# Kernel tuning notes

Hardware: AMD Instinct MI355X
Metric: run time of the kernel (lower is better)

## Reference

```python
import jax, jax.numpy as jnp
import numpy as np

DIM = 1024
NUM_HEADS = 16
HEAD_DIM = DIM // NUM_HEADS


def setup_inputs() -> dict:
    key = jax.random.key(0)
    k_x, k_q, k_k, k_v, k_o = jax.random.split(key, 5)
    B, L = 2, 2048
    scale = 1.0 / np.sqrt(DIM)
    x_bld = jax.random.normal(k_x, (B, L, DIM), dtype=jnp.float32)
    # LinearGeneral kernels: (in_features, num_heads, head_dim) for q/k/v,
    # (num_heads, head_dim, out_features) for out. Init ~ lecun_normal-ish scale.
    Wq = jax.random.normal(k_q, (DIM, NUM_HEADS, HEAD_DIM), dtype=jnp.float32) * scale
    Wk = jax.random.normal(k_k, (DIM, NUM_HEADS, HEAD_DIM), dtype=jnp.float32) * scale
    Wv = jax.random.normal(k_v, (DIM, NUM_HEADS, HEAD_DIM), dtype=jnp.float32) * scale
    Wo = jax.random.normal(k_o, (NUM_HEADS, HEAD_DIM, DIM), dtype=jnp.float32) * scale
    return {"x_bld": x_bld, "Wq": Wq, "Wk": Wk, "Wv": Wv, "Wo": Wo}


def reference(x_bld, Wq, Wk, Wv, Wo) -> jnp.ndarray:
    # Projections: [B,L,D] x [D,H,hd] -> [B,L,H,hd]
    q_blhd = jnp.einsum('bld,dhk->blhk', x_bld, Wq)
    k_blhd = jnp.einsum('bld,dhk->blhk', x_bld, Wk)
    v_blhd = jnp.einsum('bld,dhk->blhk', x_bld, Wv)
    # Scores: [B,H,L,L]
    attn_bhll = jnp.einsum('bqhd,bkhd->bhqk', q_blhd, k_blhd)
    attn_bhll = attn_bhll / jnp.sqrt(jnp.asarray(HEAD_DIM, dtype=attn_bhll.dtype))
    L = x_bld.shape[1]
    qi = jnp.arange(L)[:, None]
    ki = jnp.arange(L)[None, :]
    mask_ll = ki <= qi  # causal, no window
    neg_inf = jnp.finfo(attn_bhll.dtype).min
    attn_bhll = jnp.where(mask_ll[None, None, :, :], attn_bhll, neg_inf)
    attn_bhll = jax.nn.softmax(attn_bhll, axis=-1)
    y_blhd = jnp.einsum('bhqk,bkhd->bqhd', attn_bhll, v_blhd)
    # Output projection: contract (H, hd) -> D
    return jnp.einsum('blhk,hkd->bld', y_blhd, Wo)
```

## Files before the change

### kernel.cpp

```cpp
#include <hip/hip_runtime.h>
#include <hip/hip_bf16.h>

typedef __hip_bfloat16 bf16;
typedef __attribute__((ext_vector_type(8))) short short8;
typedef __attribute__((ext_vector_type(4))) float f32x4;

__device__ __forceinline__ float bfbits2f(unsigned short u) {
    return __uint_as_float(((unsigned int)u) << 16);
}
__device__ __forceinline__ unsigned short f2bfbits(float f) {
    union { float f; unsigned int u; } x;
    x.f = f;
    unsigned int r = x.u + 0x7FFFu + ((x.u >> 16) & 1u);
    return (unsigned short)(r >> 16);
}
__device__ __forceinline__ void async_copy16(const void* g, void* l) {
    __builtin_amdgcn_global_load_lds(
        (const __attribute__((address_space(1))) void*)g,
        (__attribute__((address_space(3))) void*)l, 16, 0, 0);
}

__global__ __launch_bounds__(256) void detect_dtype(
    const unsigned int* __restrict__ p0, const unsigned int* __restrict__ p1,
    const unsigned int* __restrict__ p2, const unsigned int* __restrict__ p3,
    const unsigned int* __restrict__ p4, int* __restrict__ flags) {
    const unsigned int* ps[5] = {p0, p1, p2, p3, p4};
    const unsigned int* p = ps[blockIdx.x];
    const int tid = threadIdx.x;
    int cnt = 0;
    for (int i = tid; i < 4096; i += 256) {
        unsigned int e = (p[i] >> 7) & 0xFFu;
        cnt += (e >= 90u && e <= 150u) ? 1 : 0;
    }
    __shared__ int r[256];
    r[tid] = cnt;
    __syncthreads();
    for (int off = 128; off; off >>= 1) {
        if (tid < off) r[tid] += r[tid + off];
        __syncthreads();
    }
    if (tid == 0) flags[blockIdx.x] = (r[0] > 2048) ? 1 : 0;
}

__global__ __launch_bounds__(256) void conv_x(const void* __restrict__ X,
                                              short* __restrict__ xb,
                                              const int* __restrict__ flags) {
    const bool isBf = flags[0] != 0;
    const int i = (blockIdx.x * 256 + threadIdx.x) * 8;
    if (isBf) {
        *(short8*)&xb[i] = *(const short8*)((const short*)X + i);
    } else {
        const float* xf = (const float*)X + i;
        float4 a = *(const float4*)xf;
        float4 b = *(const float4*)(xf + 4);
        short8 o;
        o[0] = (short)f2bfbits(a.x); o[1] = (short)f2bfbits(a.y);
        o[2] = (short)f2bfbits(a.z); o[3] = (short)f2bfbits(a.w);
        o[4] = (short)f2bfbits(b.x); o[5] = (short)f2bfbits(b.y);
        o[6] = (short)f2bfbits(b.z); o[7] = (short)f2bfbits(b.w);
        *(short8*)&xb[i] = o;
    }
}

__global__ __launch_bounds__(256) void conv_wT(
    const void* __restrict__ W1, const void* __restrict__ W2,
    const void* __restrict__ W3, const void* __restrict__ W4,
    short* __restrict__ O1, short* __restrict__ O2,
    short* __restrict__ O3, short* __restrict__ O4,
    const int* __restrict__ flags) {
    const void* Ws[4] = {W1, W2, W3, W4};
    short* Os[4] = {O1, O2, O3, O4};
    const int wsel = blockIdx.z;
    const bool isBf = flags[wsel + 1] != 0;
    const float scale = (wsel == 0) ? 0.125f : 1.0f;
    const void* W = Ws[wsel];
    short* O = Os[wsel];

    __shared__ float t[32][33];
    const int tx = threadIdx.x & 31;
    const int ty = threadIdx.x >> 5;
    const int gx = blockIdx.x * 32 + tx;
#pragma unroll
    for (int i = 0; i < 4; i++) {
        const int gy = blockIdx.y * 32 + ty + i * 8;
        float v = isBf ? bfbits2f(((const unsigned short*)W)[(size_t)gy * 1024 + gx])
                       : ((const float*)W)[(size_t)gy * 1024 + gx];
        t[ty + i * 8][tx] = v * scale;
    }
    __syncthreads();
#pragma unroll
    for (int i = 0; i < 4; i++) {
        const int orow = blockIdx.x * 32 + ty + i * 8;
        const int ocol = blockIdx.y * 32 + tx;
        O[(size_t)orow * 1024 + ocol] = (short)f2bfbits(t[tx][ty + i * 8]);
    }
}

__global__ __launch_bounds__(256) void transpose_v(const short* __restrict__ qkv,
                                                   short* __restrict__ VtG) {
    __shared__ short t[32][33];
    const int tx = threadIdx.x & 31, ty = threadIdx.x >> 5;
    const int b = blockIdx.z >> 4, h = blockIdx.z & 15;
    const int l0 = blockIdx.x * 32, d0 = blockIdx.y * 32;
#pragma unroll
    for (int i = 0; i < 4; i++) {
        const int l = l0 + ty + i * 8;
        t[ty + i * 8][tx] =
            qkv[(size_t)(b * 2048 + l) * 3072 + 2048 + h * 64 + d0 + tx];
    }
    __syncthreads();
#pragma unroll
    for (int i = 0; i < 4; i++) {
        const int d = d0 + ty + i * 8;
        VtG[((size_t)(b * 16 + h) * 64 + d) * 2048 + l0 + tx] = t[tx][ty + i * 8];
    }
}

template <int BN>
__global__ __launch_bounds__(256) void gemm_async(const short* __restrict__ A,
                                                  const short* __restrict__ Bt,
                                                  void* __restrict__ C,
                                                  const int* __restrict__ flags,
                                                  int outIdx, int M, int N, int K) {
    __shared__ short As[128 * 32];
    __shared__ short Bs[BN * 32];
    constexpr int NI = BN / 32;

    const int tid = threadIdx.x;
    const int lane = tid & 63;
    const int wv = __builtin_amdgcn_readfirstlane(tid >> 6);
    const int quad = lane >> 4, l16 = lane & 15;
    const int wr = wv >> 1, wc = wv & 1;
    const int m0 = blockIdx.y * 128, n0 = blockIdx.x * BN;

    const int gr = lane >> 2;
    const int gc = (lane & 3) * 8;

    const f32x4 zero = {0.f, 0.f, 0.f, 0.f};
    f32x4 acc[4][NI];
#pragma unroll
    for (int mi = 0; mi < 4; mi++)
#pragma unroll
        for (int ni = 0; ni < NI; ni++) acc[mi][ni] = zero;

    for (int k0 = 0; k0 < K; k0 += 32) {
#pragma unroll
        for (int t = 0; t < 2; t++) {
            const short* gp = A + (size_t)(m0 + t * 64 + wv * 16 + gr) * K + k0 + gc;
            async_copy16(gp, &As[(t * 64 + wv * 16) * 32]);
        }
#pragma unroll
        for (int t = 0; t < BN / 64; t++) {
            const short* gp = Bt + (size_t)(n0 + t * 64 + wv * 16 + gr) * K + k0 + gc;
            async_copy16(gp, &Bs[(t * 64 + wv * 16) * 32]);
        }
        __syncthreads();

        short8 af[4], bfv[NI];
#pragma unroll
        for (int mi = 0; mi < 4; mi++)
            af[mi] = *(const short8*)&As[(wr * 64 + mi * 16 + l16) * 32 + quad * 8];
#pragma unroll
        for (int ni = 0; ni < NI; ni++)
            bfv[ni] = *(const short8*)&Bs[(wc * (BN / 2) + ni * 16 + l16) * 32 + quad * 8];
#pragma unroll
        for (int mi = 0; mi < 4; mi++)
#pragma unroll
            for (int ni = 0; ni < NI; ni++)
                acc[mi][ni] = __builtin_amdgcn_mfma_f32_16x16x32_bf16(
                    af[mi], bfv[ni], acc[mi][ni], 0, 0, 0);
        __syncthreads();
    }

    const bool outBf = (outIdx < 0) ? true : (flags[outIdx] != 0);
    if (outBf) {
        unsigned short* Cb = (unsigned short*)C;
#pragma unroll
        for (int mi = 0; mi < 4; mi++)
#pragma unroll
            for (int ni = 0; ni < NI; ni++)
#pragma unroll
                for (int r = 0; r < 4; r++) {
                    const int row = m0 + wr * 64 + mi * 16 + quad * 4 + r;
                    const int col = n0 + wc * (BN / 2) + ni * 16 + l16;
                    Cb[(size_t)row * N + col] = f2bfbits(acc[mi][ni][r]);
                }
    } else {
        float* Cf = (float*)C;
#pragma unroll
        for (int mi = 0; mi < 4; mi++)
#pragma unroll
            for (int ni = 0; ni < NI; ni++)
#pragma unroll
                for (int r = 0; r < 4; r++) {
                    const int row = m0 + wr * 64 + mi * 16 + quad * 4 + r;
                    const int col = n0 + wc * (BN / 2) + ni * 16 + l16;
                    Cf[(size_t)row * N + col] = acc[mi][ni][r];
                }
    }
}

__global__ __launch_bounds__(256) void attn_mfma3(
    const short* __restrict__ qkv, const short* __restrict__ VtG,
    short* __restrict__ Yg, short* __restrict__ Opart, float2* __restrict__ ml) {
    __shared__ short Ks[2 * 128 * 32];
    __shared__ short Vt[4 * 64 * 32];
    __shared__ short Ps[4 * 64 * 32];

    const int tid = threadIdx.x;
    const int lane = tid & 63;
    const int wv = __builtin_amdgcn_readfirstlane(tid >> 6);
    const int quad = lane >> 4, l16 = lane & 15;
    const int bh = blockIdx.y;
    const int b = bh >> 4, h = bh & 15;

    int qb, seg;
    const int slot = blockIdx.x;
    if (slot < 32) { qb = 31 - (slot >> 1); seg = slot & 1; }
    else { qb = 47 - slot; seg = -1; }

    const int ns = (qb + 2) >> 1;
    int sb0, sb1;
    if (seg < 0) { sb0 = 0; sb1 = ns; }
    else {
        const int half0 = ns >> 1;
        sb0 = seg ? half0 : 0;
        sb1 = seg ? ns : half0;
    }

#pragma unroll
    for (int i = 0; i < 2; i++) {
        short* lds = &Ps[(i * 64 + wv * 16) * 32];
        const int qrow = qb * 64 + wv * 16 + (lane >> 2);
        const short* src =
            qkv + (size_t)(b * 2048 + qrow) * 3072 + h * 64 + i * 32 + (lane & 3) * 8;
        async_copy16(src, lds);
    }
    __syncthreads();
    const short8 qf0 = *(const short8*)&Ps[(wv * 16 + l16) * 32 + quad * 8];
    const short8 qf1 = *(const short8*)&Ps[(64 + wv * 16 + l16) * 32 + quad * 8];

    const f32x4 zero = {0.f, 0.f, 0.f, 0.f};
    f32x4 O[4];
#pragma unroll
    for (int ni = 0; ni < 4; ni++) O[ni] = zero;
    float m_st[4], l_st[4];
#pragma unroll
    for (int r = 0; r < 4; r++) { m_st[r] = -1e30f; l_st[r] = 0.f; }

    for (int sb = sb0; sb < sb1; sb++) {
        __syncthreads();
#pragma unroll
        for (int i = 0; i < 4; i++) {
            const int u = wv * 4 + i;
            const int half = u & 1, kr0 = (u >> 1) * 16;
            short* lds = &Ks[(half * 128 + kr0) * 32];
            const int key = sb * 128 + kr0 + (lane >> 2);
            const short* src = qkv + (size_t)(b * 2048 + key) * 3072 + 1024 +
                               h * 64 + half * 32 + (lane & 3) * 8;
            async_copy16(src, lds);
        }
#pragma unroll
        for (int i = 0; i < 4; i++) {
            const int c = i, dr0 = wv * 16;
            short* lds = &Vt[(c * 64 + dr0) * 32];
            const int d = dr0 + (lane >> 2);
            const short* src =
                VtG + ((size_t)bh * 64 + d) * 2048 + sb * 128 + c * 32 + (lane & 3) * 8;
            async_copy16(src, lds);
        }
        __syncthreads();

        f32x4 s[8];
#pragma unroll
        for (int ni = 0; ni < 8; ni++) {
            short8 kf0 = *(const short8*)&Ks[(ni * 16 + l16) * 32 + quad * 8];
            short8 kf1 = *(const short8*)&Ks[(128 + ni * 16 + l16) * 32 + quad * 8];
            s[ni] = __builtin_amdgcn_mfma_f32_16x16x32_bf16(qf0, kf0, zero, 0, 0, 0);
            s[ni] = __builtin_amdgcn_mfma_f32_16x16x32_bf16(qf1, kf1, s[ni], 0, 0, 0);
        }

        if (sb == ns - 1) {
#pragma unroll
            for (int ni = 0; ni < 8; ni++)
#pragma unroll
                for (int r = 0; r < 4; r++) {
                    const int key = sb * 128 + ni * 16 + l16;
                    const int qrow = qb * 64 + wv * 16 + quad * 4 + r;
                    if (key > qrow) s[ni][r] = -1e30f;
                }
        }

        float alpha[4];
#pragma unroll
        for (int r = 0; r < 4; r++) {
            float mb = s[0][r];
#pragma unroll
            for (int ni = 1; ni < 8; ni++) mb = fmaxf(mb, s[ni][r]);
            mb = fmaxf(mb, __shfl_xor(mb, 1));
            mb = fmaxf(mb, __shfl_xor(mb, 2));
            mb = fmaxf(mb, __shfl_xor(mb, 4));
            mb = fmaxf(mb, __shfl_xor(mb, 8));
            const float mn = fmaxf(m_st[r], mb);
            alpha[r] = __expf(m_st[r] - mn);
            m_st[r] = mn;
            float rs = 0.f;
#pragma unroll
            for (int ni = 0; ni < 8; ni++) {
                float e = __expf(s[ni][r] - mn);
                s[ni][r] = e;
                rs += e;
            }
            rs += __shfl_xor(rs, 1);
            rs += __shfl_xor(rs, 2);
            rs += __shfl_xor(rs, 4);
            rs += __shfl_xor(rs, 8);
            l_st[r] = l_st[r] * alpha[r] + rs;
            O[0][r] *= alpha[r];
            O[1][r] *= alpha[r];
            O[2][r] *= alpha[r];
            O[3][r] *= alpha[r];
        }

#pragma unroll
        for (int ni = 0; ni < 8; ni++)
#pragma unroll
            for (int r = 0; r < 4; r++)
                Ps[((ni >> 1) * 64 + wv * 16 + quad * 4 + r) * 32 +
                   (ni & 1) * 16 + l16] = (short)f2bfbits(s[ni][r]);

        short8 pf[4];
#pragma unroll
        for (int c = 0; c < 4; c++)
            pf[c] = *(const short8*)&Ps[(c * 64 + wv * 16 + l16) * 32 + quad * 8];

#pragma unroll
        for (int ni = 0; ni < 4; ni++)
#pragma unroll
            for (int c = 0; c < 4; c++) {
                short8 vf = *(const short8*)&Vt[(c * 64 + ni * 16 + l16) * 32 + quad * 8];
                O[ni] = __builtin_amdgcn_mfma_f32_16x16x32_bf16(pf[c], vf, O[ni], 0, 0, 0);
            }
    }

    if (seg < 0) {
#pragma unroll
        for (int r = 0; r < 4; r++) {
            const float inv = 1.f / l_st[r];
            const int qrow = qb * 64 + wv * 16 + quad * 4 + r;
#pragma unroll
            for (int ni = 0; ni < 4; ni++)
                Yg[(size_t)(b * 2048 + qrow) * 1024 + h * 64 + ni * 16 + l16] =
                    (short)f2bfbits(O[ni][r] * inv);
        }
    } else {
        const int qb16 = qb - 16;
        const int base = ((seg * 32 + bh) * 16 + qb16) * 64;
#pragma unroll
        for (int r = 0; r < 4; r++) {
            const int q = wv * 16 + quad * 4 + r;
            const float inv = 1.f / l_st[r];
#pragma unroll
            for (int ni = 0; ni < 4; ni++)
                Opart[(size_t)(base + q) * 64 + ni * 16 + l16] =
                    (short)f2bfbits(O[ni][r] * inv);
            if (l16 == 0) {
                float2 v; v.x = m_st[r]; v.y = l_st[r];
                ml[base + q] = v;
            }
        }
    }
}

__global__ __launch_bounds__(256) void attn_combine(
    const short* __restrict__ Opart, const float2* __restrict__ ml,
    short* __restrict__ Yg) {
    const int qb16 = blockIdx.x;
    const int bh = blockIdx.y;
    const int b = bh >> 4, h = bh & 15;
    const int tid = threadIdx.x;
    const int q = tid >> 2;
    const int d0 = (tid & 3) * 16;

    const int i0 = ((0 * 32 + bh) * 16 + qb16) * 64 + q;
    const int i1 = ((1 * 32 + bh) * 16 + qb16) * 64 + q;
    const float2 a = ml[i0], c = ml[i1];
    const float M = fmaxf(a.x, c.x);
    float w0 = __expf(a.x - M) * a.y;
    float w1 = __expf(c.x - M) * c.y;
    const float inv = 1.f / (w0 + w1);
    w0 *= inv; w1 *= inv;

    const short* p0 = Opart + (size_t)i0 * 64 + d0;
    const short* p1 = Opart + (size_t)i1 * 64 + d0;
    short8 x0 = *(const short8*)p0, y0 = *(const short8*)p1;
    short8 x1 = *(const short8*)(p0 + 8), y1 = *(const short8*)(p1 + 8);
    short8 o0, o1;
#pragma unroll
    for (int t = 0; t < 8; t++) {
        o0[t] = (short)f2bfbits(w0 * bfbits2f((unsigned short)x0[t]) +
                                w1 * bfbits2f((unsigned short)y0[t]));
        o1[t] = (short)f2bfbits(w0 * bfbits2f((unsigned short)x1[t]) +
                                w1 * bfbits2f((unsigned short)y1[t]));
    }
    const int qrow = (16 + qb16) * 64 + q;
    short* yp = Yg + (size_t)(b * 2048 + qrow) * 1024 + h * 64 + d0;
    *(short8*)yp = o0;
    *(short8*)(yp + 8) = o1;
}

extern "C" void kernel_launch(void* const* d_in, const int* in_sizes, int n_in,
                              void* d_out, int out_size, void* d_ws, size_t ws_size,
                              hipStream_t stream) {
    const int M = 2 * 2048;
    const int D = 1024;

    char* w = (char*)d_ws;
    int* flags = (int*)w;
    short* xb  = (short*)(w + 4096);
    short* WqT = (short*)(w + 4096 + (8u << 20));
    short* WkT = WqT + (1u << 20);
    short* WvT = WkT + (1u << 20);
    short* WoT = WvT + (1u << 20);
    short* qkv = WoT + (1u << 20);
    short* VtG = qkv + (size_t)M * 3072;
    short* Opart = VtG + (size_t)2048 * 2048;
    float2* mlp = (float2*)(Opart + (size_t)2 * 32 * 16 * 64 * 64);
    short* y = xb;

    detect_dtype<<<5, 256, 0, stream>>>(
        (const unsigned int*)d_in[0], (const unsigned int*)d_in[1],
        (const unsigned int*)d_in[2], (const unsigned int*)d_in[3],
        (const unsigned int*)d_in[4], flags);

    conv_x<<<2048, 256, 0, stream>>>(d_in[0], xb, flags);
    conv_wT<<<dim3(32, 32, 4), 256, 0, stream>>>(
        d_in[1], d_in[2], d_in[3], d_in[4], WqT, WkT, WvT, WoT, flags);

    gemm_async<128><<<dim3(3072 / 128, M / 128), 256, 0, stream>>>(
        xb, WqT, qkv, flags, -1, M, 3072, D);

    transpose_v<<<dim3(64, 2, 32), 256, 0, stream>>>(qkv, VtG);

    attn_mfma3<<<dim3(48, 32), 256, 0, stream>>>(qkv, VtG, y, Opart, mlp);
    attn_combine<<<dim3(16, 32), 256, 0, stream>>>(Opart, mlp, y);

    gemm_async<64><<<dim3(D / 64, M / 128), 256, 0, stream>>>(
        y, WoT, d_out, flags, 0, M, D, D);
}
```

Baseline: 223.3 us.

## Double-buffer K/V tiles in attention, swizzle P writes, reorder grid dims

The attention kernel now keeps two LDS buffers for K and V tiles and prefetches the next key block while computing on the current one, which removes one barrier per iteration and overlaps global loads with MFMA work. P stores into LDS use a rotated column index so the write pattern spreads across banks. The grid is transposed so consecutive blocks cover different heads within the same query-block slot, which changes scheduling order. The extra LDS for the double buffers may lower occupancy.

```diff
diff --git a/kernel.cpp b/kernel.cpp
--- a/kernel.cpp
+++ b/kernel.cpp
@@ -200,22 +200,22 @@
     }
 }
 
-__global__ __launch_bounds__(256) void attn_mfma3(
+__global__ __launch_bounds__(256) void attn_mfma4(
     const short* __restrict__ qkv, const short* __restrict__ VtG,
     short* __restrict__ Yg, short* __restrict__ Opart, float2* __restrict__ ml) {
-    __shared__ short Ks[2 * 128 * 32];
-    __shared__ short Vt[4 * 64 * 32];
+    __shared__ short Ks[2][2 * 128 * 32];
+    __shared__ short Vt[2][4 * 64 * 32];
     __shared__ short Ps[4 * 64 * 32];
 
     const int tid = threadIdx.x;
     const int lane = tid & 63;
     const int wv = __builtin_amdgcn_readfirstlane(tid >> 6);
     const int quad = lane >> 4, l16 = lane & 15;
-    const int bh = blockIdx.y;
+    const int bh = blockIdx.x;
     const int b = bh >> 4, h = bh & 15;
 
     int qb, seg;
-    const int slot = blockIdx.x;
+    const int slot = blockIdx.y;
     if (slot < 32) { qb = 31 - (slot >> 1); seg = slot & 1; }
     else { qb = 47 - slot; seg = -1; }
 
@@ -228,13 +228,40 @@
         sb1 = seg ? ns : half0;
     }
 
+    const int lr = lane >> 2;
+    const int lc = (lane & 3) * 8;
+    const short* kptr[4];
+    const short* vptr[4];
+    short* kdst[4];
+    short* vdst[4];
+#pragma unroll
+    for (int i = 0; i < 4; i++) {
+        const int u = wv * 4 + i;
+        const int half = u & 1, kr0 = (u >> 1) * 16;
+        kptr[i] = qkv + (size_t)(b * 2048 + sb0 * 128 + kr0 + lr) * 3072 + 1024 +
+                  h * 64 + half * 32 + lc;
+        kdst[i] = &Ks[0][(half * 128 + kr0) * 32];
+        vptr[i] = VtG + ((size_t)bh * 64 + wv * 16 + lr) * 2048 + sb0 * 128 +
+                  i * 32 + lc;
+        vdst[i] = &Vt[0][(i * 64 + wv * 16) * 32];
+    }
+    const int kbufoff = (int)(&Ks[1][0] - &Ks[0][0]);
+    const int vbufoff = (int)(&Vt[1][0] - &Vt[0][0]);
+    const int buf0 = sb0 & 1;
+
 #pragma unroll
     for (int i = 0; i < 2; i++) {
-        short* lds = &Ps[(i * 64 + wv * 16) * 32];
-        const int qrow = qb * 64 + wv * 16 + (lane >> 2);
+        const int qrow = qb * 64 + wv * 16 + lr;
         const short* src =
-            qkv + (size_t)(b * 2048 + qrow) * 3072 + h * 64 + i * 32 + (lane & 3) * 8;
-        async_copy16(src, lds);
+            qkv + (size_t)(b * 2048 + qrow) * 3072 + h * 64 + i * 32 + lc;
+        async_copy16(src, &Ps[(i * 64 + wv * 16) * 32]);
+    }
+#pragma unroll
+    for (int i = 0; i < 4; i++) {
+        async_copy16(kptr[i], kdst[i] + buf0 * kbufoff);
+        async_copy16(vptr[i], vdst[i] + buf0 * vbufoff);
+        kptr[i] += 128 * 3072;
+        vptr[i] += 128;
     }
     __syncthreads();
     const short8 qf0 = *(const short8*)&Ps[(wv * 16 + l16) * 32 + quad * 8];
@@ -248,50 +275,44 @@
 #pragma unroll
     for (int r = 0; r < 4; r++) { m_st[r] = -1e30f; l_st[r] = 0.f; }
 
+    const int qrow0 = qb * 64 + wv * 16 + quad * 4;
+    const int protA = ((quad + (l16 >> 2)) & 3) * 8;
+
     for (int sb = sb0; sb < sb1; sb++) {
-        __syncthreads();
-#pragma unroll
-        for (int i = 0; i < 4; i++) {
-            const int u = wv * 4 + i;
-            const int half = u & 1, kr0 = (u >> 1) * 16;
-            short* lds = &Ks[(half * 128 + kr0) * 32];
-            const int key = sb * 128 + kr0 + (lane >> 2);
-            const short* src = qkv + (size_t)(b * 2048 + key) * 3072 + 1024 +
-                               h * 64 + half * 32 + (lane & 3) * 8;
-            async_copy16(src, lds);
-        }
-#pragma unroll
-        for (int i = 0; i < 4; i++) {
-            const int c = i, dr0 = wv * 16;
-            short* lds = &Vt[(c * 64 + dr0) * 32];
-            const int d = dr0 + (lane >> 2);
-            const short* src =
-                VtG + ((size_t)bh * 64 + d) * 2048 + sb * 128 + c * 32 + (lane & 3) * 8;
-            async_copy16(src, lds);
-        }
-        __syncthreads();
+        const int cur = sb & 1;
+        if (sb != sb0) __syncthreads();
+        if (sb + 1 < sb1) {
+            const int nxt = cur ^ 1;
+#pragma unroll
+            for (int i = 0; i < 4; i++) {
+                async_copy16(kptr[i], kdst[i] + nxt * kbufoff);
+                async_copy16(vptr[i], vdst[i] + nxt * vbufoff);
+                kptr[i] += 128 * 3072;
+                vptr[i] += 128;
+            }
+        }
+        const short* Kc = &Ks[0][0] + cur * kbufoff;
+        const short* Vc = &Vt[0][0] + cur * vbufoff;
 
         f32x4 s[8];
 #pragma unroll
         for (int ni = 0; ni < 8; ni++) {
-            short8 kf0 = *(const short8*)&Ks[(ni * 16 + l16) * 32 + quad * 8];
-            short8 kf1 = *(const short8*)&Ks[(128 + ni * 16 + l16) * 32 + quad * 8];
+            short8 kf0 = *(const short8*)&Kc[(ni * 16 + l16) * 32 + quad * 8];
+            short8 kf1 = *(const short8*)&Kc[(128 + ni * 16 + l16) * 32 + quad * 8];
             s[ni] = __builtin_amdgcn_mfma_f32_16x16x32_bf16(qf0, kf0, zero, 0, 0, 0);
             s[ni] = __builtin_amdgcn_mfma_f32_16x16x32_bf16(qf1, kf1, s[ni], 0, 0, 0);
         }
 
         if (sb == ns - 1) {
 #pragma unroll
-            for (int ni = 0; ni < 8; ni++)
-#pragma unroll
-                for (int r = 0; r < 4; r++) {
-                    const int key = sb * 128 + ni * 16 + l16;
-                    const int qrow = qb * 64 + wv * 16 + quad * 4 + r;
-                    if (key > qrow) s[ni][r] = -1e30f;
-                }
-        }
-
-        float alpha[4];
+            for (int ni = 0; ni < 8; ni++) {
+                const int key = sb * 128 + ni * 16 + l16;
+#pragma unroll
+                for (int r = 0; r < 4; r++)
+                    if (key > qrow0 + r) s[ni][r] = -1e30f;
+            }
+        }
+
 #pragma unroll
         for (int r = 0; r < 4; r++) {
             float mb = s[0][r];
@@ -302,7 +323,7 @@
             mb = fmaxf(mb, __shfl_xor(mb, 4));
             mb = fmaxf(mb, __shfl_xor(mb, 8));
             const float mn = fmaxf(m_st[r], mb);
-            alpha[r] = __expf(m_st[r] - mn);
+            const float alpha = __expf(m_st[r] - mn);
             m_st[r] = mn;
             float rs = 0.f;
 #pragma unroll
@@ -315,30 +336,31 @@
             rs += __shfl_xor(rs, 2);
             rs += __shfl_xor(rs, 4);
             rs += __shfl_xor(rs, 8);
-            l_st[r] = l_st[r] * alpha[r] + rs;
-            O[0][r] *= alpha[r];
-            O[1][r] *= alpha[r];
-            O[2][r] *= alpha[r];
-            O[3][r] *= alpha[r];
-        }
-
-#pragma unroll
-        for (int ni = 0; ni < 8; ni++)
+            l_st[r] = l_st[r] * alpha + rs;
+            O[0][r] *= alpha;
+            O[1][r] *= alpha;
+            O[2][r] *= alpha;
+            O[3][r] *= alpha;
+        }
+
+#pragma unroll
+        for (int ni = 0; ni < 8; ni++) {
+            const int colr = (((ni & 1) * 16 + l16) + quad * 8) & 31;
 #pragma unroll
             for (int r = 0; r < 4; r++)
-                Ps[((ni >> 1) * 64 + wv * 16 + quad * 4 + r) * 32 +
-                   (ni & 1) * 16 + l16] = (short)f2bfbits(s[ni][r]);
-
+                Ps[((ni >> 1) * 64 + wv * 16 + quad * 4 + r) * 32 + colr] =
+                    (short)f2bfbits(s[ni][r]);
+        }
         short8 pf[4];
 #pragma unroll
         for (int c = 0; c < 4; c++)
-            pf[c] = *(const short8*)&Ps[(c * 64 + wv * 16 + l16) * 32 + quad * 8];
+            pf[c] = *(const short8*)&Ps[(c * 64 + wv * 16 + l16) * 32 + protA];
 
 #pragma unroll
         for (int ni = 0; ni < 4; ni++)
 #pragma unroll
             for (int c = 0; c < 4; c++) {
-                short8 vf = *(const short8*)&Vt[(c * 64 + ni * 16 + l16) * 32 + quad * 8];
+                short8 vf = *(const short8*)&Vc[(c * 64 + ni * 16 + l16) * 32 + quad * 8];
                 O[ni] = __builtin_amdgcn_mfma_f32_16x16x32_bf16(pf[c], vf, O[ni], 0, 0, 0);
             }
     }
@@ -347,7 +369,7 @@
 #pragma unroll
         for (int r = 0; r < 4; r++) {
             const float inv = 1.f / l_st[r];
-            const int qrow = qb * 64 + wv * 16 + quad * 4 + r;
+            const int qrow = qrow0 + r;
 #pragma unroll
             for (int ni = 0; ni < 4; ni++)
                 Yg[(size_t)(b * 2048 + qrow) * 1024 + h * 64 + ni * 16 + l16] =
@@ -442,7 +464,7 @@
 
     transpose_v<<<dim3(64, 2, 32), 256, 0, stream>>>(qkv, VtG);
 
-    attn_mfma3<<<dim3(48, 32), 256, 0, stream>>>(qkv, VtG, y, Opart, mlp);
+    attn_mfma4<<<dim3(32, 48), 256, 0, stream>>>(qkv, VtG, y, Opart, mlp);
     attn_combine<<<dim3(16, 32), 256, 0, stream>>>(Opart, mlp, y);
 
     gemm_async<64><<<dim3(D / 64, M / 128), 256, 0, stream>>>(
```

New measurement: 221.3 us. About the same (-0.9%).
